# Kernel optimization log

Hardware: AMD Instinct MI355X
Metric: run time of the kernel (lower is better)

## Reference

```python
import jax, jax.numpy as jnp
import numpy as np
from jax import lax

# PRPN constants (match init_kwargs)
NSLOTS = 15
NLOOKBACK = 1
RESOLUTION = 0.1
NLAYERS = 2
H = 1024      # nhid == ninp
NTOKEN = 32000
T, B = 256, 64
INF = 1e8


def masked_softmax(x, mask):
    # PRPN blocks.softmax: exp-normalize then multiply by gate mask
    e = jnp.exp(x - jnp.max(x, axis=-1, keepdims=True))
    e = e * mask
    return e / (jnp.sum(e, axis=-1, keepdims=True) + 1e-8)


def setup_inputs() -> dict:
    key = jax.random.key(0)
    ks = jax.random.split(key, 16)
    s = 0.02
    return {
        'tokens': jax.random.randint(ks[0], (T, B), 0, NTOKEN),
        'emb_table': s * jax.random.normal(ks[1], (NTOKEN, H), jnp.float32),
        'conv1_w': s * jax.random.normal(ks[2], (H, H, NLOOKBACK + 1), jnp.float32),
        'conv1_b': jnp.zeros((H,), jnp.float32),
        'bn1_gamma': jnp.ones((H,), jnp.float32),
        'bn1_beta': jnp.zeros((H,), jnp.float32),
        'conv2_w': s * jax.random.normal(ks[3], (2, H // 2, 1), jnp.float32),
        'conv2_b': jnp.zeros((2,), jnp.float32),
        'reader_wih': s * jax.random.normal(ks[4], (NLAYERS, 4 * H, H), jnp.float32),
        'reader_whh': s * jax.random.normal(ks[5], (NLAYERS, 4 * H, H), jnp.float32),
        'reader_bih': jnp.zeros((NLAYERS, 4 * H), jnp.float32),
        'reader_bhh': jnp.zeros((NLAYERS, 4 * H), jnp.float32),
        'reader_summ_w': s * jax.random.normal(ks[6], (NLAYERS, H, 2 * H), jnp.float32),
        'reader_summ_b': jnp.zeros((NLAYERS, H), jnp.float32),
        'pred_summ_w': s * jax.random.normal(ks[7], (H, 2 * H), jnp.float32),
        'pred_summ_b': jnp.zeros((H,), jnp.float32),
        'ffd_w': s * jax.random.normal(ks[8], (H, 2 * H), jnp.float32),
        'ffd_b': jnp.zeros((H,), jnp.float32),
        'ffd_gamma': jnp.ones((H,), jnp.float32),
        'ffd_beta': jnp.zeros((H,), jnp.float32),
    }


def _parser_gates(emb, conv1_w, conv1_b, bn1_gamma, bn1_beta, conv2_w, conv2_b):
    # emb: (T, B, H). Parser state init: zeros lookback embs, +inf cum_gate.
    t = emb.shape[0]
    emb_last = jnp.concatenate([jnp.zeros((NLOOKBACK,) + emb.shape[1:], emb.dtype), emb], axis=0)
    x = jnp.transpose(emb_last, (1, 2, 0))  # (B, H, T+lookback)
    h = lax.conv_general_dilated(x, conv1_w, (1,), 'VALID',
                                 dimension_numbers=('NCH', 'OIH', 'NCH'))
    h = h + conv1_b[None, :, None]
    h = bn1_gamma[None, :, None] * h + bn1_beta[None, :, None]  # BatchNorm1d (eval, mean=0,var=1)
    h = jax.nn.relu(h)
    g = lax.conv_general_dilated(h, conv2_w, (1,), 'VALID', feature_group_count=2,
                                 dimension_numbers=('NCH', 'OIH', 'NCH'))
    g = jax.nn.sigmoid(g + conv2_b[None, :, None])  # (B, 2, T)
    gate, gate_next = g[:, 0], g[:, 1]  # (B, T)
    cum_gate = jnp.concatenate([jnp.full((gate.shape[0], NSLOTS), INF, gate.dtype), gate], axis=1)
    # gate_hat[:, t, j] = cum_gate[:, (NSLOTS - j) + t], slots stacked for i = NSLOTS..1
    idx = jnp.arange(t)[:, None] + (NSLOTS - jnp.arange(NSLOTS))[None, :]
    gate_hat = cum_gate[:, idx]  # (B, T, NSLOTS)
    mg = jnp.cumprod(jax.nn.sigmoid((gate[:, :, None] - gate_hat) / RESOLUTION * 10 + 5), axis=2)
    mgn = jnp.cumprod(jax.nn.sigmoid((gate_next[:, :, None] - gate_hat) / RESOLUTION * 10 + 5), axis=2)
    return mg, mgn  # (B, T, NSLOTS)


def _prpn_forward(tokens, emb_table, conv1_w, conv1_b, bn1_gamma, bn1_beta, conv2_w, conv2_b,
                  reader_wih, reader_whh, reader_bih, reader_bhh, reader_summ_w, reader_summ_b,
                  pred_summ_w, pred_summ_b, ffd_w, ffd_b, ffd_gamma, ffd_beta):
    t, b = tokens.shape
    emb = emb_table[tokens]  # (T, B, H)
    mg, mgn = _parser_gates(emb, conv1_w, conv1_b, bn1_gamma, bn1_beta, conv2_w, conv2_b)
    mg_t = jnp.transpose(mg, (1, 0, 2))   # (T, B, S)
    mgn_t = jnp.transpose(mgn, (1, 0, 2))
    inv_sqrt_h = 1.0 / np.sqrt(H).astype(np.float32)

    def step(carry, xs):
        rh, rc, pm = carry  # (L,B,S,H), (L,B,S,H), (B,S,H)
        emb_i, mg_i, mgn_i = xs
        h = emb_i
        new_rh, new_rc = [], []
        for j in range(NLAYERS):
            mh, mc = rh[j], rc[j]
            key = jnp.concatenate([h, mh[:, -1]], axis=1) @ reader_summ_w[j].T + reader_summ_b[j]
            logits = jnp.einsum('bsh,bh->bs', mh, key) * inv_sqrt_h
            att = masked_softmax(logits, mg_i)
            sel_h = jnp.einsum('bs,bsh->bh', att, mh)
            sel_c = jnp.einsum('bs,bsh->bh', att, mc)
            gates = h @ reader_wih[j].T + reader_bih[j] + sel_h @ reader_whh[j].T + reader_bhh[j]
            ig, fg, gg, og = jnp.split(gates, 4, axis=1)
            c_new = jax.nn.sigmoid(fg) * sel_c + jax.nn.sigmoid(ig) * jnp.tanh(gg)
            h = jax.nn.sigmoid(og) * jnp.tanh(c_new)
            new_rh.append(jnp.concatenate([mh[:, 1:], h[:, None]], axis=1))
            new_rc.append(jnp.concatenate([mc[:, 1:], c_new[:, None]], axis=1))
        # predictor attention over its own slot memory, gated by memory_gate_next
        key = jnp.concatenate([h, pm[:, -1]], axis=1) @ pred_summ_w.T + pred_summ_b
        logits = jnp.einsum('bsh,bh->bs', pm, key) * inv_sqrt_h
        att = masked_softmax(logits, mgn_i)
        sel = jnp.einsum('bs,bsh->bh', att, pm)
        pm = jnp.concatenate([pm[:, 1:], h[:, None]], axis=1)
        return (jnp.stack(new_rh), jnp.stack(new_rc), pm), (h, sel)

    z = jnp.zeros((NLAYERS, b, NSLOTS, H), emb.dtype)
    carry0 = (z, z, jnp.zeros((b, NSLOTS, H), emb.dtype))
    _, (hs, sels) = lax.scan(step, carry0, (emb, mg_t, mgn_t))
    x = jnp.concatenate([hs.reshape(-1, H), sels.reshape(-1, H)], axis=1)  # (T*B, 2H)
    out = jnp.tanh(ffd_gamma * (x @ ffd_w.T + ffd_b) + ffd_beta)  # PredictNetwork.ffd (BN eval)
    return out


def reference(tokens, emb_table, conv1_w, conv1_b, bn1_gamma, bn1_beta, conv2_w, conv2_b,
              reader_wih, reader_whh, reader_bih, reader_bhh, reader_summ_w, reader_summ_b,
              pred_summ_w, pred_summ_b, ffd_w, ffd_b, ffd_gamma, ffd_beta):
    out = _prpn_forward(tokens, emb_table, conv1_w, conv1_b, bn1_gamma, bn1_beta, conv2_w, conv2_b,
                        reader_wih, reader_whh, reader_bih, reader_bhh, reader_summ_w, reader_summ_b,
                        pred_summ_w, pred_summ_b, ffd_w, ffd_b, ffd_gamma, ffd_beta)
    mask = tokens != 0
    return out, mask
```

## Files before the change

### kernel.cpp

```cpp
#include <hip/hip_runtime.h>


typedef _Float16 half8 __attribute__((ext_vector_type(8)));
typedef float f32x4 __attribute__((ext_vector_type(4)));

#define LSTR 56

__device__ __forceinline__ float sigm(float x) { return 1.0f / (1.0f + expf(-x)); }

__device__ __forceinline__ void store_ct(float* p, float v)    { *p = v; }
__device__ __forceinline__ void store_ct(_Float16* p, float v) { *p = (_Float16)v; }

__device__ __forceinline__ void mfma_loop(const _Float16* __restrict__ Ag, int lda,
                                          const _Float16* __restrict__ Bg, int ldb,
                                          int K, _Float16* As, _Float16* Bs, f32x4* acc)
{
  const int tid = threadIdx.x;
  const int lr  = tid >> 2;
  const int lc  = (tid & 3) << 3;
  const int ln  = tid & 63;
  const int wv  = tid >> 6;
  const int m15 = ln & 15;
  const int q   = ln >> 4;
  const _Float16* ap = Ag + (size_t)lr * lda + lc;
  const _Float16* bp = Bg + (size_t)lr * ldb + lc;
  _Float16* asw = As + lr * LSTR + lc;
  _Float16* bsw = Bs + lr * LSTR + lc;
  const _Float16* asr = As + (wv * 16 + m15) * LSTR + q * 8;
  const _Float16* bsr = Bs + m15 * LSTR + q * 8;
  for (int k0 = 0; k0 < K; k0 += 32) {
    half8 av = *(const half8*)(ap); ap += 32;
    half8 bv = *(const half8*)(bp); bp += 32;
    __syncthreads();
    *(half8*)asw = av;
    *(half8*)bsw = bv;
    __syncthreads();
    half8 a = *(const half8*)asr;
#pragma unroll
    for (int j = 0; j < 4; j++) {
      half8 b = *(const half8*)(bsr + j * 16 * LSTR);
      acc[j] = __builtin_amdgcn_mfma_f32_16x16x32_f16(a, b, acc[j], 0, 0, 0);
    }
  }
}

template <int ACT, typename CT>
__global__ __launch_bounds__(256) void gemm_bt(const _Float16* __restrict__ A, int lda,
                                               const _Float16* __restrict__ B, int ldb,
                                               CT* __restrict__ C, int ldc, int K,
                                               const float* __restrict__ p0,
                                               const float* __restrict__ p1,
                                               const float* __restrict__ p2)
{
  __shared__ __align__(16) _Float16 As[64 * LSTR];
  __shared__ __align__(16) _Float16 Bs[64 * LSTR];
  f32x4 acc[4] = {};
  const int ntile = blockIdx.x, mtile = blockIdx.y;
  mfma_loop(A + (size_t)mtile * 64 * lda, lda, B + (size_t)ntile * 64 * ldb, ldb, K, As, Bs, acc);
  const int ln = threadIdx.x & 63, wv = threadIdx.x >> 6;
  const int m15 = ln & 15, q = ln >> 4;
#pragma unroll
  for (int j = 0; j < 4; j++) {
    const int col = ntile * 64 + j * 16 + m15;
    float b0 = 0.f, b1 = 0.f, b2 = 0.f;
    if (ACT == 0) {
      if (p0) b0 = p0[col];
      if (p1) b0 += p1[col];
    } else {
      b0 = p0[col]; b1 = p1[col]; b2 = p2[col];
    }
#pragma unroll
    for (int r = 0; r < 4; r++) {
      const int row = mtile * 64 + wv * 16 + q * 4 + r;
      float v = acc[j][r];
      if (ACT == 0) v += b0;
      else {
        v = b0 * (v + b1) + b2;
        v = (ACT == 1) ? fmaxf(v, 0.f) : tanhf(v);
      }
      store_ct(&C[(size_t)row * ldc + col], v);
    }
  }
}

struct Seg {
  const _Float16* B; float* C; const float* b1; const float* b2;
  int ldb; int ldc; int tile0;
};
struct BundleArgs { Seg s[4]; };

__global__ __launch_bounds__(256) void k_bundle(const _Float16* __restrict__ A, BundleArgs args)
{
  __shared__ __align__(16) _Float16 As[64 * LSTR];
  __shared__ __align__(16) _Float16 Bs[64 * LSTR];
  f32x4 acc[4] = {};
  const int bt = blockIdx.x;
  int si = 0;
  if (bt >= args.s[1].tile0) si = 1;
  if (bt >= args.s[2].tile0) si = 2;
  if (bt >= args.s[3].tile0) si = 3;
  Seg sg = args.s[si];
  const int ntile = bt - sg.tile0;
  mfma_loop(A, 1024, sg.B + (size_t)ntile * 64 * sg.ldb, sg.ldb, 1024, As, Bs, acc);
  const int ln = threadIdx.x & 63, wv = threadIdx.x >> 6;
  const int m15 = ln & 15, q = ln >> 4;
#pragma unroll
  for (int j = 0; j < 4; j++) {
    const int col = ntile * 64 + j * 16 + m15;
    float bb = 0.f;
    if (sg.b1) bb += sg.b1[col];
    if (sg.b2) bb += sg.b2[col];
#pragma unroll
    for (int r = 0; r < 4; r++) {
      const int row = wv * 16 + q * 4 + r;
      sg.C[(size_t)row * sg.ldc + col] = acc[j][r] + bb;
    }
  }
}

template <typename KT, typename GT>
__global__ __launch_bounds__(256) void k_cell(
    const KT* __restrict__ keyA, const float* __restrict__ keyB,
    const GT* __restrict__ gatesIn,
    const float* __restrict__ ringH, float* __restrict__ ringC,
    const float* __restrict__ proj, const float* __restrict__ mask,
    float* __restrict__ hOut, float* __restrict__ cOut,
    _Float16* __restrict__ hHalf, int t)
{
  const int b = blockIdx.x, tid = threadIdx.x;
  __shared__ float s_key[1024];
  __shared__ float s_att[16];
  for (int i = tid; i < 1024; i += 256)
    s_key[i] = (float)keyA[b * 1024 + i] + keyB[b * 1024 + i];
  __syncthreads();
  const int wv = tid >> 6, ln = tid & 63;
  for (int s = wv; s < 15; s += 4) {
    const float* hr = ringH + ((size_t)((t + s) % 15) * 64 + b) * 1024;
    float p = 0.f;
    for (int i = ln; i < 1024; i += 64) p = fmaf(hr[i], s_key[i], p);
    for (int off = 32; off > 0; off >>= 1) p += __shfl_down(p, off, 64);
    if (ln == 0) s_att[s] = p * 0.03125f;
  }
  __syncthreads();
  if (tid == 0) {
    float mx = -1e30f;
    for (int s = 0; s < 15; s++) mx = fmaxf(mx, s_att[s]);
    float den = 1e-8f, e[15];
    for (int s = 0; s < 15; s++) { e[s] = expf(s_att[s] - mx) * mask[b * 15 + s]; den += e[s]; }
    float inv = 1.f / den;
    for (int s = 0; s < 15; s++) s_att[s] = e[s] * inv;
  }
  __syncthreads();
  float att[15];
  int poff[15], coff[15];
#pragma unroll
  for (int s = 0; s < 15; s++) {
    att[s] = s_att[s];
    int ph = (t + s) % 15;
    poff[s] = ph * 262144 + b * 4096;
    coff[s] = ph * 65536 + b * 1024;
  }
  for (int c = tid; c < 1024; c += 256) {
    float g[4];
#pragma unroll
    for (int gi = 0; gi < 4; gi++) {
      const int gidx = gi * 1024 + c;
      float a = (float)gatesIn[(size_t)b * 4096 + gidx];
      for (int s = 0; s < 15; s++) a = fmaf(att[s], proj[(size_t)poff[s] + gidx], a);
      g[gi] = a;
    }
    float selc = 0.f;
    for (int s = 0; s < 15; s++) selc = fmaf(att[s], ringC[(size_t)coff[s] + c], selc);
    const float ig = sigm(g[0]), fg = sigm(g[1]), gg = tanhf(g[2]), og = sigm(g[3]);
    const float cn = fg * selc + ig * gg;
    const float h  = og * tanhf(cn);
    cOut[b * 1024 + c]  = cn;
    hOut[b * 1024 + c]  = h;
    hHalf[b * 1024 + c] = (_Float16)h;
  }
}

__global__ __launch_bounds__(256) void k_pred(
    const float* __restrict__ keyA, const float* __restrict__ keyB,
    const float* __restrict__ ringH, const float* __restrict__ mask,
    const float* __restrict__ h1buf, float* __restrict__ ringW,
    _Float16* __restrict__ xrow, int t)
{
  const int b = blockIdx.x, tid = threadIdx.x;
  __shared__ float s_key[1024];
  __shared__ float s_att[16];
  for (int i = tid; i < 1024; i += 256)
    s_key[i] = keyA[b * 1024 + i] + keyB[b * 1024 + i];
  __syncthreads();
  const int wv = tid >> 6, ln = tid & 63;
  for (int s = wv; s < 15; s += 4) {
    const float* hr = ringH + ((size_t)((t + s) % 15) * 64 + b) * 1024;
    float p = 0.f;
    for (int i = ln; i < 1024; i += 64) p = fmaf(hr[i], s_key[i], p);
    for (int off = 32; off > 0; off >>= 1) p += __shfl_down(p, off, 64);
    if (ln == 0) s_att[s] = p * 0.03125f;
  }
  __syncthreads();
  if (tid == 0) {
    float mx = -1e30f;
    for (int s = 0; s < 15; s++) mx = fmaxf(mx, s_att[s]);
    float den = 1e-8f, e[15];
    for (int s = 0; s < 15; s++) { e[s] = expf(s_att[s] - mx) * mask[b * 15 + s]; den += e[s]; }
    float inv = 1.f / den;
    for (int s = 0; s < 15; s++) s_att[s] = e[s] * inv;
  }
  __syncthreads();
  float att[15];
  int coff[15];
#pragma unroll
  for (int s = 0; s < 15; s++) { att[s] = s_att[s]; coff[s] = ((t + s) % 15) * 65536 + b * 1024; }
  for (int c = tid; c < 1024; c += 256) {
    float sel = 0.f;
    for (int s = 0; s < 15; s++) sel = fmaf(att[s], ringH[(size_t)coff[s] + c], sel);
    const float h = h1buf[b * 1024 + c];
    ringW[b * 1024 + c] = h;
    xrow[(size_t)b * 2048 + c]        = (_Float16)h;
    xrow[(size_t)b * 2048 + 1024 + c] = (_Float16)sel;
  }
}

__global__ void k_zero(float* __restrict__ p, int n) {
  int i = blockIdx.x * 256 + threadIdx.x;
  const int st = gridDim.x * 256;
  for (; i < n; i += st) p[i] = 0.f;
}

__global__ void k_cvt(const float* __restrict__ s, _Float16* __restrict__ d, int n) {
  int i = blockIdx.x * 256 + threadIdx.x;
  const int st = gridDim.x * 256;
  for (; i < n; i += st) d[i] = (_Float16)s[i];
}

__global__ void k_w1r(const float* __restrict__ w, _Float16* __restrict__ d) {
  const int i = blockIdx.x * 256 + threadIdx.x;
  if (i >= 2097152) return;
  const int o = i >> 11, kk = i & 2047;
  const int src = (kk < 1024) ? (o * 2048 + kk * 2) : (o * 2048 + (kk - 1024) * 2 + 1);
  d[i] = (_Float16)w[src];
}

__global__ void k_emb(const int* __restrict__ tokens, const float* __restrict__ table,
                      _Float16* __restrict__ embpair, float* __restrict__ maskOut)
{
  const int tb = blockIdx.x;
  const int t = tb >> 6, b = tb & 63;
  const int tok = tokens[tb];
  const float* row = table + (size_t)tok * 1024;
  _Float16* dst1 = embpair + (size_t)tb * 2048 + 1024;
  for (int i = threadIdx.x; i < 1024; i += 256) {
    const _Float16 v = (_Float16)row[i];
    dst1[i] = v;
    if (t + 1 < 256) embpair[(size_t)(tb + 64) * 2048 + i] = v;
    if (t == 0)      embpair[(size_t)b * 2048 + i] = (_Float16)0.f;
  }
  if (threadIdx.x == 0) maskOut[tb] = (tok != 0) ? 1.f : 0.f;
}

__global__ __launch_bounds__(128) void k_conv2(const _Float16* __restrict__ hcv,
                                               const float* __restrict__ w2, const float* __restrict__ b2,
                                               float* __restrict__ gate, float* __restrict__ gaten)
{
  const int r = blockIdx.x;
  const int wv = threadIdx.x >> 6, ln = threadIdx.x & 63;
  const _Float16* hr = hcv + (size_t)r * 1024 + wv * 512;
  const float* wr = w2 + wv * 512;
  float p = 0.f;
  for (int i = ln; i < 512; i += 64) p = fmaf((float)hr[i], wr[i], p);
  for (int off = 32; off > 0; off >>= 1) p += __shfl_down(p, off, 64);
  if (ln == 0) {
    const float v = sigm(p + b2[wv]);
    (wv ? gaten : gate)[r] = v;
  }
}

__global__ void k_masks(const float* __restrict__ gate, const float* __restrict__ gaten,
                        float* __restrict__ mg, float* __restrict__ mgn)
{
  const int i = blockIdx.x * 256 + threadIdx.x;
  if (i >= 16384) return;
  const int t = i >> 6, b = i & 63;
  const float gc = gate[i], gn = gaten[i];
  float p = 1.f, q = 1.f;
  for (int s = 0; s < 15; s++) {
    const float gh = (s <= t) ? gate[(t - s) * 64 + b] : 1e8f;
    p *= sigm((gc - gh) * 100.f + 5.f);
    q *= sigm((gn - gh) * 100.f + 5.f);
    mg[(size_t)i * 15 + s] = p;
    mgn[(size_t)i * 15 + s] = q;
  }
}

extern "C" void kernel_launch(void* const* d_in, const int* in_sizes, int n_in,
                              void* d_out, int out_size, void* d_ws, size_t ws_size,
                              hipStream_t stream)
{
  (void)in_sizes; (void)n_in; (void)out_size; (void)ws_size;
  const int*   tokens = (const int*)d_in[0];
  const float* table  = (const float*)d_in[1];
  const float* w1     = (const float*)d_in[2];
  const float* c1b    = (const float*)d_in[3];
  const float* g1     = (const float*)d_in[4];
  const float* bt1    = (const float*)d_in[5];
  const float* w2     = (const float*)d_in[6];
  const float* c2b    = (const float*)d_in[7];
  const float* wih    = (const float*)d_in[8];
  const float* whh    = (const float*)d_in[9];
  const float* bih    = (const float*)d_in[10];
  const float* bhh    = (const float*)d_in[11];
  const float* wsm    = (const float*)d_in[12];
  const float* bsm    = (const float*)d_in[13];
  const float* wpd    = (const float*)d_in[14];
  const float* bpd    = (const float*)d_in[15];
  const float* ffw    = (const float*)d_in[16];
  const float* ffb    = (const float*)d_in[17];
  const float* ffg    = (const float*)d_in[18];
  const float* ffbt   = (const float*)d_in[19];

  float* outp    = (float*)d_out;
  float* maskOut = outp + 16777216;

  char* wp_ = (char*)d_ws;
  auto alloc = [&](size_t b) { void* r = (void*)wp_; wp_ += (b + 255) & ~(size_t)255; return r; };

  _Float16* embpair  = (_Float16*)alloc(67108864);
  _Float16* hcv      = (_Float16*)alloc(33554432);
  _Float16* embgates = (_Float16*)alloc(134217728);
  _Float16* wihF     = (_Float16*)alloc(16777216);
  _Float16* whhF     = (_Float16*)alloc(16777216);
  _Float16* wsmF     = (_Float16*)alloc(8388608);
  _Float16* wpdF     = (_Float16*)alloc(4194304);
  _Float16* ffwF     = (_Float16*)alloc(4194304);
  _Float16* w1rF     = (_Float16*)alloc(4194304);
  _Float16* h0h      = (_Float16*)alloc(131072);
  _Float16* h1h      = (_Float16*)alloc(131072);
  float* gate    = (float*)alloc(65536);
  float* gaten   = (float*)alloc(65536);
  float* mg      = (float*)alloc(983040);
  float* mgn     = (float*)alloc(983040);
  float* key1s   = (float*)alloc(262144);
  float* gates1i = (float*)alloc(1048576);
  float* keypred = (float*)alloc(262144);
  float* h1buf   = (float*)alloc(262144);
  float* zb = (float*)alloc(48234496);
  float* ringH0 = zb;
  float* ringC0 = ringH0 + 983040;
  float* ringH1 = ringC0 + 983040;
  float* ringC1 = ringH1 + 983040;
  float* P0     = ringC1 + 983040;
  float* P1     = P0 + 3932160;
  float* kc0    = P1 + 3932160;
  float* kc1    = kc0 + 65536;
  float* kcp0   = kc1 + 65536;
  float* kcp1   = kcp0 + 65536;

  _Float16* xbuf   = embpair;
  _Float16* embkey = hcv;

  k_zero<<<4096, 256, 0, stream>>>(zb, 12058624);
  k_emb<<<16384, 256, 0, stream>>>(tokens, table, embpair, maskOut);
  k_cvt<<<8192, 256, 0, stream>>>(wih, wihF, 8388608);
  k_cvt<<<8192, 256, 0, stream>>>(whh, whhF, 8388608);
  k_cvt<<<8192, 256, 0, stream>>>(wsm, wsmF, 4194304);
  k_cvt<<<4096, 256, 0, stream>>>(wpd, wpdF, 2097152);
  k_cvt<<<4096, 256, 0, stream>>>(ffw, ffwF, 2097152);
  k_w1r<<<8192, 256, 0, stream>>>(w1, w1rF);
  gemm_bt<1, _Float16><<<dim3(16, 256), 256, 0, stream>>>(embpair, 2048, w1rF, 2048, hcv, 1024, 2048, g1, c1b, bt1);
  k_conv2<<<16384, 128, 0, stream>>>(hcv, w2, c2b, gate, gaten);
  k_masks<<<64, 256, 0, stream>>>(gate, gaten, mg, mgn);
  gemm_bt<0, _Float16><<<dim3(64, 256), 256, 0, stream>>>(embpair + 1024, 2048, wihF, 1024, embgates, 4096, 1024, bih, bhh, nullptr);
  gemm_bt<0, _Float16><<<dim3(16, 256), 256, 0, stream>>>(embpair + 1024, 2048, wsmF, 2048, embkey, 1024, 1024, bsm, nullptr, nullptr);

  for (int t = 0; t < 256; ++t) {
    const int physw = t % 15;
    float* kcpW = (t & 1) ? kcp1 : kcp0;
    float* kcpR = (t & 1) ? kcp0 : kcp1;

    k_cell<_Float16, _Float16><<<64, 256, 0, stream>>>(
        embkey + (size_t)t * 65536, kc0, embgates + (size_t)t * 262144,
        ringH0, ringC0, P0, mg + (size_t)t * 960,
        ringH0 + (size_t)physw * 65536, ringC0 + (size_t)physw * 65536, h0h, t);

    {
      BundleArgs a;
      a.s[0] = { whhF,                 P0 + (size_t)physw * 262144, nullptr,    nullptr,    1024, 4096, 0   };
      a.s[1] = { wsmF + 1024,          kc0,                         nullptr,    nullptr,    2048, 1024, 64  };
      a.s[2] = { wihF + 4194304,       gates1i,                     bih + 4096, bhh + 4096, 1024, 4096, 80  };
      a.s[3] = { wsmF + 2097152,       key1s,                       bsm + 1024, nullptr,    2048, 1024, 144 };
      k_bundle<<<160, 256, 0, stream>>>(h0h, a);
    }

    k_cell<float, float><<<64, 256, 0, stream>>>(
        key1s, kc1, gates1i,
        ringH1, ringC1, P1, mg + (size_t)t * 960,
        h1buf, ringC1 + (size_t)physw * 65536, h1h, t);

    {
      BundleArgs a;
      a.s[0] = { whhF + 4194304,        P1 + (size_t)physw * 262144, nullptr, nullptr, 1024, 4096, 0  };
      a.s[1] = { wsmF + 2097152 + 1024, kc1,                         nullptr, nullptr, 2048, 1024, 64 };
      a.s[2] = { wpdF,                  keypred,                     bpd,     nullptr, 2048, 1024, 80 };
      a.s[3] = { wpdF + 1024,           kcpW,                        nullptr, nullptr, 2048, 1024, 96 };
      k_bundle<<<112, 256, 0, stream>>>(h1h, a);
    }

    k_pred<<<64, 256, 0, stream>>>(
        keypred, kcpR, ringH1, mgn + (size_t)t * 960, h1buf,
        ringH1 + (size_t)physw * 65536, xbuf + (size_t)t * 131072, t);
  }

  gemm_bt<2, float><<<dim3(16, 256), 256, 0, stream>>>(xbuf, 2048, ffwF, 2048, outp, 1024, 2048, ffg, ffb, ffbt);
}
```

Before: 29.82 ms.

## Fuse per-timestep recurrent kernels into one persistent kernel with grid barriers

Replaces the 5 kernel launches per timestep (cell, bundle GEMM, cell, bundle GEMM, pred) with a single persistent 256-block kernel that uses atomic-flag grid barriers between phases. It overlaps work by running the next step's layer-0 cell alongside the layer-1 GEMMs, and the previous step's pred alongside the layer-0 GEMMs. Ring buffers grow from 15 to 16 slots so modulo becomes a bitmask, and the MFMA loop now prefetches the next global tile before compute. The intent is to remove launch latency and idle gaps across 1280 launches. In exchange it relies on all blocks being co-resident and pays spin-barrier cost on every phase.

```diff
diff --git a/kernel.cpp b/kernel.cpp
--- a/kernel.cpp
+++ b/kernel.cpp
@@ -28,13 +28,18 @@
   _Float16* bsw = Bs + lr * LSTR + lc;
   const _Float16* asr = As + (wv * 16 + m15) * LSTR + q * 8;
   const _Float16* bsr = Bs + m15 * LSTR + q * 8;
+  half8 av = *(const half8*)ap;
+  half8 bv = *(const half8*)bp;
   for (int k0 = 0; k0 < K; k0 += 32) {
-    half8 av = *(const half8*)(ap); ap += 32;
-    half8 bv = *(const half8*)(bp); bp += 32;
     __syncthreads();
     *(half8*)asw = av;
     *(half8*)bsw = bv;
     __syncthreads();
+    if (k0 + 32 < K) {
+      ap += 32; bp += 32;
+      av = *(const half8*)ap;
+      bv = *(const half8*)bp;
+    }
     half8 a = *(const half8*)asr;
 #pragma unroll
     for (int j = 0; j < 4; j++) {
@@ -83,24 +88,12 @@
   }
 }
 
-struct Seg {
-  const _Float16* B; float* C; const float* b1; const float* b2;
-  int ldb; int ldc; int tile0;
-};
-struct BundleArgs { Seg s[4]; };
-
-__global__ __launch_bounds__(256) void k_bundle(const _Float16* __restrict__ A, BundleArgs args)
-{
-  __shared__ __align__(16) _Float16 As[64 * LSTR];
-  __shared__ __align__(16) _Float16 Bs[64 * LSTR];
+struct SegP { const _Float16* B; float* C; const float* b1; const float* b2; int ldb; int ldc; };
+
+__device__ void bundle_tile(const _Float16* __restrict__ A, const SegP sg, int ntile,
+                            _Float16* As, _Float16* Bs)
+{
   f32x4 acc[4] = {};
-  const int bt = blockIdx.x;
-  int si = 0;
-  if (bt >= args.s[1].tile0) si = 1;
-  if (bt >= args.s[2].tile0) si = 2;
-  if (bt >= args.s[3].tile0) si = 3;
-  Seg sg = args.s[si];
-  const int ntile = bt - sg.tile0;
   mfma_loop(A, 1024, sg.B + (size_t)ntile * 64 * sg.ldb, sg.ldb, 1024, As, Bs, acc);
   const int ln = threadIdx.x & 63, wv = threadIdx.x >> 6;
   const int m15 = ln & 15, q = ln >> 4;
@@ -119,23 +112,21 @@
 }
 
 template <typename KT, typename GT>
-__global__ __launch_bounds__(256) void k_cell(
+__device__ void cell_body(int b, int c0, int nch, int t,
     const KT* __restrict__ keyA, const float* __restrict__ keyB,
     const GT* __restrict__ gatesIn,
-    const float* __restrict__ ringH, float* __restrict__ ringC,
+    const float* __restrict__ ringH, const float* __restrict__ ringC,
     const float* __restrict__ proj, const float* __restrict__ mask,
-    float* __restrict__ hOut, float* __restrict__ cOut,
-    _Float16* __restrict__ hHalf, int t)
-{
-  const int b = blockIdx.x, tid = threadIdx.x;
-  __shared__ float s_key[1024];
-  __shared__ float s_att[16];
+    float* __restrict__ hRingOut, float* __restrict__ cRingOut,
+    _Float16* __restrict__ hHalf, float* s_key, float* s_att)
+{
+  const int tid = threadIdx.x;
   for (int i = tid; i < 1024; i += 256)
     s_key[i] = (float)keyA[b * 1024 + i] + keyB[b * 1024 + i];
   __syncthreads();
   const int wv = tid >> 6, ln = tid & 63;
   for (int s = wv; s < 15; s += 4) {
-    const float* hr = ringH + ((size_t)((t + s) % 15) * 64 + b) * 1024;
+    const float* hr = ringH + ((size_t)((t + s) & 15) * 64 + b) * 1024;
     float p = 0.f;
     for (int i = ln; i < 1024; i += 64) p = fmaf(hr[i], s_key[i], p);
     for (int off = 32; off > 0; off >>= 1) p += __shfl_down(p, off, 64);
@@ -156,11 +147,11 @@
 #pragma unroll
   for (int s = 0; s < 15; s++) {
     att[s] = s_att[s];
-    int ph = (t + s) % 15;
-    poff[s] = ph * 262144 + b * 4096;
-    coff[s] = ph * 65536 + b * 1024;
-  }
-  for (int c = tid; c < 1024; c += 256) {
+    const int phs = (t + s) & 15;
+    poff[s] = phs * 262144 + b * 4096;
+    coff[s] = phs * 65536 + b * 1024;
+  }
+  for (int c = c0 + tid; c < c0 + nch; c += 256) {
     float g[4];
 #pragma unroll
     for (int gi = 0; gi < 4; gi++) {
@@ -174,27 +165,24 @@
     const float ig = sigm(g[0]), fg = sigm(g[1]), gg = tanhf(g[2]), og = sigm(g[3]);
     const float cn = fg * selc + ig * gg;
     const float h  = og * tanhf(cn);
-    cOut[b * 1024 + c]  = cn;
-    hOut[b * 1024 + c]  = h;
-    hHalf[b * 1024 + c] = (_Float16)h;
-  }
-}
-
-__global__ __launch_bounds__(256) void k_pred(
+    cRingOut[b * 1024 + c] = cn;
+    hRingOut[b * 1024 + c] = h;
+    hHalf[b * 1024 + c]    = (_Float16)h;
+  }
+}
+
+__device__ void pred_body(int b, int c0, int nch, int t,
     const float* __restrict__ keyA, const float* __restrict__ keyB,
     const float* __restrict__ ringH, const float* __restrict__ mask,
-    const float* __restrict__ h1buf, float* __restrict__ ringW,
-    _Float16* __restrict__ xrow, int t)
-{
-  const int b = blockIdx.x, tid = threadIdx.x;
-  __shared__ float s_key[1024];
-  __shared__ float s_att[16];
+    _Float16* __restrict__ xrow, float* s_key, float* s_att)
+{
+  const int tid = threadIdx.x;
   for (int i = tid; i < 1024; i += 256)
     s_key[i] = keyA[b * 1024 + i] + keyB[b * 1024 + i];
   __syncthreads();
   const int wv = tid >> 6, ln = tid & 63;
   for (int s = wv; s < 15; s += 4) {
-    const float* hr = ringH + ((size_t)((t + s) % 15) * 64 + b) * 1024;
+    const float* hr = ringH + ((size_t)((t + s) & 15) * 64 + b) * 1024;
     float p = 0.f;
     for (int i = ln; i < 1024; i += 64) p = fmaf(hr[i], s_key[i], p);
     for (int off = 32; off > 0; off >>= 1) p += __shfl_down(p, off, 64);
@@ -211,17 +199,108 @@
   }
   __syncthreads();
   float att[15];
-  int coff[15];
-#pragma unroll
-  for (int s = 0; s < 15; s++) { att[s] = s_att[s]; coff[s] = ((t + s) % 15) * 65536 + b * 1024; }
-  for (int c = tid; c < 1024; c += 256) {
+  int hoff[15];
+#pragma unroll
+  for (int s = 0; s < 15; s++) { att[s] = s_att[s]; hoff[s] = ((t + s) & 15) * 65536 + b * 1024; }
+  const float* hNew = ringH + (size_t)((t + 15) & 15) * 65536 + b * 1024;
+  for (int c = c0 + tid; c < c0 + nch; c += 256) {
     float sel = 0.f;
-    for (int s = 0; s < 15; s++) sel = fmaf(att[s], ringH[(size_t)coff[s] + c], sel);
-    const float h = h1buf[b * 1024 + c];
-    ringW[b * 1024 + c] = h;
+    for (int s = 0; s < 15; s++) sel = fmaf(att[s], ringH[(size_t)hoff[s] + c], sel);
+    const float h = hNew[c];
     xrow[(size_t)b * 2048 + c]        = (_Float16)h;
     xrow[(size_t)b * 2048 + 1024 + c] = (_Float16)sel;
   }
+}
+
+__device__ __forceinline__ void gsync(unsigned* arrive, unsigned* release, unsigned ph, int bid)
+{
+  __syncthreads();
+  const int tid = threadIdx.x;
+  if (bid == 0) {
+    if (tid >= 1) {
+      while (__hip_atomic_load(&arrive[tid << 5], __ATOMIC_RELAXED, __HIP_MEMORY_SCOPE_AGENT) < ph)
+        __builtin_amdgcn_s_sleep(1);
+    }
+    __syncthreads();
+    if (tid == 0) {
+      __threadfence();
+      __hip_atomic_store(release, ph, __ATOMIC_RELAXED, __HIP_MEMORY_SCOPE_AGENT);
+    }
+    __syncthreads();
+  } else {
+    if (tid == 0) {
+      __threadfence();
+      __hip_atomic_store(&arrive[bid << 5], ph, __ATOMIC_RELAXED, __HIP_MEMORY_SCOPE_AGENT);
+      while (__hip_atomic_load(release, __ATOMIC_RELAXED, __HIP_MEMORY_SCOPE_AGENT) < ph)
+        __builtin_amdgcn_s_sleep(1);
+      __threadfence();
+    }
+    __syncthreads();
+  }
+}
+
+struct ScanArgs {
+  const _Float16 *embkey, *embgates, *wihF, *whhF, *wsmF, *wpdF;
+  const float *mg, *mgn, *bih, *bhh, *bsm, *bpd;
+  float *ringH0, *ringC0, *ringH1, *ringC1, *P0, *P1;
+  float *kc0, *kc1, *kcp0, *kcp1, *key1s, *gates1i, *keypred;
+  _Float16 *h0h, *h1h, *xbuf;
+  unsigned *bar;
+};
+
+__global__ __launch_bounds__(256, 1) void k_scan(ScanArgs A)
+{
+  __shared__ __align__(16) _Float16 As[64 * LSTR];
+  __shared__ __align__(16) _Float16 Bs[64 * LSTR];
+  float* s_key = (float*)As;
+  float* s_att = (float*)Bs;
+  const int bid = blockIdx.x;
+  unsigned* arrive  = A.bar;
+  unsigned* release = A.bar + 8192;
+  unsigned ph = 0;
+
+  cell_body<_Float16, _Float16>(bid >> 2, (bid & 3) << 8, 256, 0,
+      A.embkey, A.kc0, A.embgates, A.ringH0, A.ringC0, A.P0, A.mg,
+      A.ringH0 + (size_t)15 * 65536, A.ringC0 + (size_t)15 * 65536, A.h0h, s_key, s_att);
+  gsync(arrive, release, ++ph, bid);
+
+  for (int t = 0; t < 256; ++t) {
+    const int w15 = (t + 15) & 15;
+    if (bid < 160) {
+      SegP sg; int nt;
+      if (bid < 64)       { sg = SegP{A.whhF,                 A.P0 + (size_t)w15 * 262144, nullptr,      nullptr,      1024, 4096}; nt = bid; }
+      else if (bid < 80)  { sg = SegP{A.wsmF + 1024,          A.kc0,                       nullptr,      nullptr,      2048, 1024}; nt = bid - 64; }
+      else if (bid < 144) { sg = SegP{A.wihF + 4194304,       A.gates1i,                   A.bih + 4096, A.bhh + 4096, 1024, 4096}; nt = bid - 80; }
+      else                { sg = SegP{A.wsmF + 2097152,       A.key1s,                     A.bsm + 1024, nullptr,      2048, 1024}; nt = bid - 144; }
+      bundle_tile(A.h0h, sg, nt, As, Bs);
+    } else if (bid < 224 && t > 0) {
+      pred_body(bid - 160, 0, 1024, t - 1, A.keypred, ((t - 1) & 1) ? A.kcp0 : A.kcp1,
+                A.ringH1, A.mgn + (size_t)(t - 1) * 960, A.xbuf + (size_t)(t - 1) * 131072, s_key, s_att);
+    }
+    gsync(arrive, release, ++ph, bid);
+    cell_body<float, float>(bid >> 2, (bid & 3) << 8, 256, t,
+        A.key1s, A.kc1, A.gates1i, A.ringH1, A.ringC1, A.P1, A.mg + (size_t)t * 960,
+        A.ringH1 + (size_t)w15 * 65536, A.ringC1 + (size_t)w15 * 65536, A.h1h, s_key, s_att);
+    gsync(arrive, release, ++ph, bid);
+    if (bid < 112) {
+      SegP sg; int nt;
+      float* kcpW = (t & 1) ? A.kcp1 : A.kcp0;
+      if (bid < 64)       { sg = SegP{A.whhF + 4194304,        A.P1 + (size_t)w15 * 262144, nullptr, nullptr, 1024, 4096}; nt = bid; }
+      else if (bid < 80)  { sg = SegP{A.wsmF + 2097152 + 1024, A.kc1,                       nullptr, nullptr, 2048, 1024}; nt = bid - 64; }
+      else if (bid < 96)  { sg = SegP{A.wpdF,                  A.keypred,                   A.bpd,   nullptr, 2048, 1024}; nt = bid - 80; }
+      else                { sg = SegP{A.wpdF + 1024,           kcpW,                        nullptr, nullptr, 2048, 1024}; nt = bid - 96; }
+      bundle_tile(A.h1h, sg, nt, As, Bs);
+    } else if (bid < 240 && t < 255) {
+      const int bb = (bid - 112) >> 1, c0 = ((bid - 112) & 1) << 9;
+      cell_body<_Float16, _Float16>(bb, c0, 512, t + 1,
+          A.embkey + (size_t)(t + 1) * 65536, A.kc0, A.embgates + (size_t)(t + 1) * 262144,
+          A.ringH0, A.ringC0, A.P0, A.mg + (size_t)(t + 1) * 960,
+          A.ringH0 + (size_t)(t & 15) * 65536, A.ringC0 + (size_t)(t & 15) * 65536, A.h0h, s_key, s_att);
+    }
+    gsync(arrive, release, ++ph, bid);
+  }
+  pred_body(bid >> 2, (bid & 3) << 8, 256, 255, A.keypred, A.kcp0,
+            A.ringH1, A.mgn + (size_t)255 * 960, A.xbuf + (size_t)255 * 131072, s_key, s_att);
 }
 
 __global__ void k_zero(float* __restrict__ p, int n) {
@@ -345,23 +424,23 @@
   float* key1s   = (float*)alloc(262144);
   float* gates1i = (float*)alloc(1048576);
   float* keypred = (float*)alloc(262144);
-  float* h1buf   = (float*)alloc(262144);
-  float* zb = (float*)alloc(48234496);
+  float* zb = (float*)alloc(51413120);
   float* ringH0 = zb;
-  float* ringC0 = ringH0 + 983040;
-  float* ringH1 = ringC0 + 983040;
-  float* ringC1 = ringH1 + 983040;
-  float* P0     = ringC1 + 983040;
-  float* P1     = P0 + 3932160;
-  float* kc0    = P1 + 3932160;
+  float* ringC0 = ringH0 + 1048576;
+  float* ringH1 = ringC0 + 1048576;
+  float* ringC1 = ringH1 + 1048576;
+  float* P0     = ringC1 + 1048576;
+  float* P1     = P0 + 4194304;
+  float* kc0    = P1 + 4194304;
   float* kc1    = kc0 + 65536;
   float* kcp0   = kc1 + 65536;
   float* kcp1   = kcp0 + 65536;
+  unsigned* bar = (unsigned*)(kcp1 + 65536);
 
   _Float16* xbuf   = embpair;
   _Float16* embkey = hcv;
 
-  k_zero<<<4096, 256, 0, stream>>>(zb, 12058624);
+  k_zero<<<4096, 256, 0, stream>>>(zb, 12853280);
   k_emb<<<16384, 256, 0, stream>>>(tokens, table, embpair, maskOut);
   k_cvt<<<8192, 256, 0, stream>>>(wih, wihF, 8388608);
   k_cvt<<<8192, 256, 0, stream>>>(whh, whhF, 8388608);
@@ -375,43 +454,17 @@
   gemm_bt<0, _Float16><<<dim3(64, 256), 256, 0, stream>>>(embpair + 1024, 2048, wihF, 1024, embgates, 4096, 1024, bih, bhh, nullptr);
   gemm_bt<0, _Float16><<<dim3(16, 256), 256, 0, stream>>>(embpair + 1024, 2048, wsmF, 2048, embkey, 1024, 1024, bsm, nullptr, nullptr);
 
-  for (int t = 0; t < 256; ++t) {
-    const int physw = t % 15;
-    float* kcpW = (t & 1) ? kcp1 : kcp0;
-    float* kcpR = (t & 1) ? kcp0 : kcp1;
-
-    k_cell<_Float16, _Float16><<<64, 256, 0, stream>>>(
-        embkey + (size_t)t * 65536, kc0, embgates + (size_t)t * 262144,
-        ringH0, ringC0, P0, mg + (size_t)t * 960,
-        ringH0 + (size_t)physw * 65536, ringC0 + (size_t)physw * 65536, h0h, t);
-
-    {
-      BundleArgs a;
-      a.s[0] = { whhF,                 P0 + (size_t)physw * 262144, nullptr,    nullptr,    1024, 4096, 0   };
-      a.s[1] = { wsmF + 1024,          kc0,                         nullptr,    nullptr,    2048, 1024, 64  };
-      a.s[2] = { wihF + 4194304,       gates1i,                     bih + 4096, bhh + 4096, 1024, 4096, 80  };
-      a.s[3] = { wsmF + 2097152,       key1s,                       bsm + 1024, nullptr,    2048, 1024, 144 };
-      k_bundle<<<160, 256, 0, stream>>>(h0h, a);
-    }
-
-    k_cell<float, float><<<64, 256, 0, stream>>>(
-        key1s, kc1, gates1i,
-        ringH1, ringC1, P1, mg + (size_t)t * 960,
-        h1buf, ringC1 + (size_t)physw * 65536, h1h, t);
-
-    {
-      BundleArgs a;
-      a.s[0] = { whhF + 4194304,        P1 + (size_t)physw * 262144, nullptr, nullptr, 1024, 4096, 0  };
-      a.s[1] = { wsmF + 2097152 + 1024, kc1,                         nullptr, nullptr, 2048, 1024, 64 };
-      a.s[2] = { wpdF,                  keypred,                     bpd,     nullptr, 2048, 1024, 80 };
-      a.s[3] = { wpdF + 1024,           kcpW,                        nullptr, nullptr, 2048, 1024, 96 };
-      k_bundle<<<112, 256, 0, stream>>>(h1h, a);
-    }
-
-    k_pred<<<64, 256, 0, stream>>>(
-        keypred, kcpR, ringH1, mgn + (size_t)t * 960, h1buf,
-        ringH1 + (size_t)physw * 65536, xbuf + (size_t)t * 131072, t);
-  }
+  ScanArgs sa;
+  sa.embkey = embkey; sa.embgates = embgates;
+  sa.wihF = wihF; sa.whhF = whhF; sa.wsmF = wsmF; sa.wpdF = wpdF;
+  sa.mg = mg; sa.mgn = mgn; sa.bih = bih; sa.bhh = bhh; sa.bsm = bsm; sa.bpd = bpd;
+  sa.ringH0 = ringH0; sa.ringC0 = ringC0; sa.ringH1 = ringH1; sa.ringC1 = ringC1;
+  sa.P0 = P0; sa.P1 = P1;
+  sa.kc0 = kc0; sa.kc1 = kc1; sa.kcp0 = kcp0; sa.kcp1 = kcp1;
+  sa.key1s = key1s; sa.gates1i = gates1i; sa.keypred = keypred;
+  sa.h0h = h0h; sa.h1h = h1h; sa.xbuf = xbuf;
+  sa.bar = bar;
+  k_scan<<<dim3(256), dim3(256), 0, stream>>>(sa);
 
   gemm_bt<2, float><<<dim3(16, 256), 256, 0, stream>>>(xbuf, 2048, ffwF, 2048, outp, 1024, 2048, ffg, ffb, ffbt);
 }
```

New measurement: 29.07 ms. 2.5% less time.
